# Kernel tuning notes

Measured on AMD Instinct MI355X. Metric: run time of the kernel, lower is better.

## Reference

```python
import jax, jax.numpy as jnp
import numpy as np

B, N, E = 32, 256, 300   # batch, num hyperedges, word emb size
H, K = 256, 8            # nhidden, nhead
MARGIN = 0.2


def setup_inputs() -> dict:
    key = jax.random.key(0)
    ks = jax.random.split(key, 10)
    s_in = 1.0 / np.sqrt(E)
    s_h = 1.0 / np.sqrt(H)
    s_fc = 1.0 / np.sqrt(H * K)
    return {
        'he_anchor': jax.random.normal(ks[0], (B, N, E), jnp.float32),
        'he_pos': jax.random.normal(ks[1], (B, N, E), jnp.float32),
        'he_neg': jax.random.normal(ks[2], (B, N, E), jnp.float32),
        'W_a2h': jax.random.uniform(ks[3], (H, E), jnp.float32, -s_in, s_in),
        'b_a2h': jax.random.uniform(ks[4], (H,), jnp.float32, -s_in, s_in),
        'W_c2h': jax.random.uniform(ks[5], (H, E), jnp.float32, -s_in, s_in),
        'b_c2h': jax.random.uniform(ks[6], (H,), jnp.float32, -s_in, s_in),
        'W_att': jax.random.uniform(ks[7], (K, H), jnp.float32, -s_h, s_h),
        'b_att': jax.random.uniform(ks[8], (K,), jnp.float32, -s_h, s_h),
        'W_fc': jax.random.uniform(ks[9], (1, H * K), jnp.float32, -s_fc, s_fc),
        'b_fc': jnp.zeros((1,), jnp.float32),
    }


def _score(x, y, W_a2h, b_a2h, W_c2h, b_c2h, W_att, b_att, W_fc, b_fc):
    # a2h / c2h projections, then permute to [B, H, N]
    Aa = jnp.transpose(x @ W_a2h.T + b_a2h, (0, 2, 1))  # [B,H,N]
    Ac = jnp.transpose(y @ W_c2h.T + b_c2h, (0, 2, 1))  # [B,H,M]
    # h2att applied to the outer product Aa[b,h,n]*Ac[b,h,m]; fuse into one einsum
    logits = jnp.einsum('bhn,bhm,kh->bknm', Aa, Ac, W_att) + b_att[None, :, None, None]
    b_, k_, n_, m_ = logits.shape
    att = jax.nn.softmax(logits.reshape(b_, k_, n_ * m_), axis=-1).reshape(b_, k_, n_, m_)
    # per-head bilinear aggregation: out[b,k,h] = sum_{n,m} Aa[b,h,n]*att[b,k,n,m]*Ac[b,h,m]
    t = jnp.einsum('bhn,bknm->bkhm', Aa, att)
    out = jnp.einsum('bkhm,bhm->bkh', t, Ac)
    # torch concat order is head-major: [B, K*H]
    out = out.reshape(b_, k_ * H)
    return out @ W_fc.T + b_fc  # [B,1]


def reference(he_anchor, he_pos, he_neg, W_a2h, b_a2h, W_c2h, b_c2h, W_att, b_att, W_fc, b_fc):
    score_p = _score(he_anchor, he_pos, W_a2h, b_a2h, W_c2h, b_c2h, W_att, b_att, W_fc, b_fc)
    score_n = _score(he_anchor, he_neg, W_a2h, b_a2h, W_c2h, b_c2h, W_att, b_att, W_fc, b_fc)
    loss = jnp.mean(jax.nn.relu(score_n - score_p + MARGIN))
    return loss
```

## Files before the change

kernel.cpp:

```cpp
#include <hip/hip_runtime.h>

#define BB 32
#define NN 256
#define EE 300
#define HH 256
#define KK 8
#define MARGINF 0.2f
#define EP 320

typedef __attribute__((ext_vector_type(8))) short bf16x8;
typedef __attribute__((ext_vector_type(4))) float f32x4;
typedef __attribute__((ext_vector_type(16))) float f32x16;

__device__ inline ushort f2bf(float f) {
  unsigned u = __float_as_uint(f);
  u += 0x7fffu + ((u >> 16) & 1u);
  return (ushort)(u >> 16);
}
__device__ inline float bf2f(ushort s) { return __uint_as_float(((unsigned)s) << 16); }
__device__ inline unsigned pack2bf(float f0, float f1) {
  unsigned u0 = __float_as_uint(f0); u0 += 0x7fffu + ((u0 >> 16) & 1u);
  unsigned u1 = __float_as_uint(f1); u1 += 0x7fffu + ((u1 >> 16) & 1u);
  return (u0 >> 16) | (u1 & 0xffff0000u);
}

__global__ __launch_bounds__(256) void wconv_kernel(
    const float* __restrict__ Wa, const float* __restrict__ Wc,
    ushort* __restrict__ Wb)
{
  const int i = blockIdx.x * 256 + threadIdx.x;
  const int e = i % EP;
  const int hw = i / EP;
  const int h = hw & 255;
  const int w = hw >> 8;
  const float* src = w ? Wc : Wa;
  Wb[i] = (e < EE) ? f2bf(src[(size_t)h * EE + e]) : (ushort)0;
}

__global__ __launch_bounds__(256, 3) void proj_kernel(
    const float* __restrict__ he_a, const float* __restrict__ he_p,
    const float* __restrict__ he_n, const ushort* __restrict__ Wb,
    const float* __restrict__ b_a2h, const float* __restrict__ b_c2h,
    ushort* __restrict__ AT)
{
  const int z = blockIdx.y;
  const int which = z >> 5;
  const int b = z & 31;
  const int n0 = blockIdx.x * 32;
  const int tid = threadIdx.x;
  const int wv = tid >> 6;
  const int lane = tid & 63;
  const int col = lane & 15;
  const int quad = lane >> 4;

  const float* X = (which == 0 ? he_a : which == 1 ? he_p : he_n) + (size_t)b * NN * EE;
  const ushort* W = Wb + (size_t)(which == 0 ? 0 : 1) * HH * EP;
  const float* bias = (which == 0 ? b_a2h : b_c2h);

  __shared__ __align__(16) ushort sX[32][328];
  __shared__ __align__(16) ushort tr[32][264];

  {
    const int row = tid >> 3, seg = tid & 7;
    const float* xr = X + (size_t)(n0 + row) * EE;
#pragma unroll
    for (int q = 0; q < 10; q++) {
      const int j = seg + 8 * q;
      float4 xv = {0.f, 0.f, 0.f, 0.f};
      if (j < 75) xv = *(const float4*)&xr[4 * j];
      uint2 p; p.x = pack2bf(xv.x, xv.y); p.y = pack2bf(xv.z, xv.w);
      *(uint2*)&sX[row][4 * j] = p;
    }
  }
  __syncthreads();

  f32x4 acc[2][4];
#pragma unroll
  for (int nf = 0; nf < 2; nf++)
#pragma unroll
    for (int mb = 0; mb < 4; mb++) acc[nf][mb] = (f32x4){0.f, 0.f, 0.f, 0.f};

#pragma unroll
  for (int ks = 0; ks < 10; ks++) {
    const int off = 32 * ks + 8 * quad;
    const bf16x8 a0 = *(const bf16x8*)&sX[col][off];
    const bf16x8 a1 = *(const bf16x8*)&sX[16 + col][off];
#pragma unroll
    for (int mb = 0; mb < 4; mb++) {
      const bf16x8 w8 = *(const bf16x8*)&W[(size_t)(64 * wv + 16 * mb + col) * EP + off];
      acc[0][mb] = __builtin_amdgcn_mfma_f32_16x16x32_bf16(a0, w8, acc[0][mb], 0, 0, 0);
      acc[1][mb] = __builtin_amdgcn_mfma_f32_16x16x32_bf16(a1, w8, acc[1][mb], 0, 0, 0);
    }
  }

#pragma unroll
  for (int nf = 0; nf < 2; nf++)
#pragma unroll
    for (int mb = 0; mb < 4; mb++) {
      const float bi = bias[64 * wv + 16 * mb + col];
#pragma unroll
      for (int r = 0; r < 4; r++)
        tr[16 * nf + 4 * quad + r][64 * wv + 16 * mb + col] = f2bf(acc[nf][mb][r] + bi);
    }
  __syncthreads();
  {
    const int row = tid >> 3, seg = tid & 7;
    ushort* dst = &AT[((size_t)(which * BB + b) * NN + n0 + row) * HH];
#pragma unroll
    for (int j = 0; j < 4; j++)
      *(uint4*)&dst[(seg * 4 + j) * 8] = *(const uint4*)&tr[row][(seg * 4 + j) * 8];
  }
}

__global__ __launch_bounds__(256, 2) void attn_kernel(
    const ushort* __restrict__ AT, const float* __restrict__ Watt,
    const float* __restrict__ Wfc, float* __restrict__ scoresK)
{
  const int idx = blockIdx.x;
  const int k = idx >> 6;
  const int g = idx & 63;
  const int which = g >> 5;
  const int b = g & 31;
  const int tid = threadIdx.x;
  const int wv = tid >> 6;
  const int lane = tid & 63;
  const int row32 = lane & 31;
  const int half32 = lane >> 5;

  const ushort* At_a = AT + (size_t)b * NN * HH;
  const ushort* At_c = AT + ((size_t)(1 + which) * BB + b) * NN * HH;
  const uint4* Ac_u4 = (const uint4*)At_c;

  __shared__ __align__(16) ushort sAc[64][264];
  __shared__ __align__(16) float wkf[256];
  __shared__ __align__(16) float wff[256];
  __shared__ float red[8];

  wkf[tid] = Watt[(size_t)k * HH + tid];
  wff[tid] = Wfc[(size_t)k * HH + tid];
  __syncthreads();

  float num = 0.f, den = 0.f;
  const int srow = tid >> 5, scol8 = (tid & 31) * 8;

  for (int s = 0; s < 2; s++) {
    const int nbase = 128 * s + 32 * wv;
    bf16x8 saf[16], gaf[16];
    const ushort* arow = At_a + (size_t)(nbase + row32) * HH;
#pragma unroll
    for (int ks = 0; ks < 16; ks++) {
      const int off = 16 * ks + 8 * half32;
      const bf16x8 a = *(const bf16x8*)&arow[off];
      const float4 wa = *(const float4*)&wkf[off];
      const float4 wb = *(const float4*)&wkf[off + 4];
      const float4 fa = *(const float4*)&wff[off];
      const float4 fb = *(const float4*)&wff[off + 4];
      const float w[8] = {wa.x, wa.y, wa.z, wa.w, wb.x, wb.y, wb.z, wb.w};
      const float f[8] = {fa.x, fa.y, fa.z, fa.w, fb.x, fb.y, fb.z, fb.w};
      union { bf16x8 v; unsigned u[4]; } sv, gv;
#pragma unroll
      for (int jj = 0; jj < 4; jj++) {
        const float a0 = bf2f((ushort)a[2 * jj]), a1 = bf2f((ushort)a[2 * jj + 1]);
        sv.u[jj] = pack2bf(a0 * w[2 * jj], a1 * w[2 * jj + 1]);
        gv.u[jj] = pack2bf(a0 * f[2 * jj], a1 * f[2 * jj + 1]);
      }
      saf[ks] = sv.v; gaf[ks] = gv.v;
    }

    for (int mc = 0; mc < 4; mc++) {
      __syncthreads();
#pragma unroll
      for (int q = 0; q < 8; q++) {
        const int row = q * 8 + srow;
        *(uint4*)&sAc[row][scol8] = Ac_u4[(size_t)(64 * mc + row) * 32 + (tid & 31)];
      }
      __syncthreads();

      f32x16 aS0 = {0,0,0,0,0,0,0,0,0,0,0,0,0,0,0,0};
      f32x16 aS1 = {0,0,0,0,0,0,0,0,0,0,0,0,0,0,0,0};
      f32x16 aG0 = {0,0,0,0,0,0,0,0,0,0,0,0,0,0,0,0};
      f32x16 aG1 = {0,0,0,0,0,0,0,0,0,0,0,0,0,0,0,0};
#pragma unroll
      for (int ks = 0; ks < 16; ks++) {
        const int off = 16 * ks + 8 * half32;
        const bf16x8 b0 = *(const bf16x8*)&sAc[row32][off];
        const bf16x8 b1 = *(const bf16x8*)&sAc[32 + row32][off];
        aS0 = __builtin_amdgcn_mfma_f32_32x32x16_bf16(saf[ks], b0, aS0, 0, 0, 0);
        aG0 = __builtin_amdgcn_mfma_f32_32x32x16_bf16(gaf[ks], b0, aG0, 0, 0, 0);
        aS1 = __builtin_amdgcn_mfma_f32_32x32x16_bf16(saf[ks], b1, aS1, 0, 0, 0);
        aG1 = __builtin_amdgcn_mfma_f32_32x32x16_bf16(gaf[ks], b1, aG1, 0, 0, 0);
      }
#pragma unroll
      for (int r = 0; r < 16; r++) {
        const float p0 = __expf(aS0[r]);
        den += p0; num += p0 * aG0[r];
        const float p1 = __expf(aS1[r]);
        den += p1; num += p1 * aG1[r];
      }
    }
  }

#pragma unroll
  for (int off = 32; off >= 1; off >>= 1) {
    num += __shfl_xor(num, off);
    den += __shfl_xor(den, off);
  }
  if (lane == 0) { red[wv] = num; red[4 + wv] = den; }
  __syncthreads();
  if (tid == 0) {
    const float nt = red[0] + red[1] + red[2] + red[3];
    const float dt = red[4] + red[5] + red[6] + red[7];
    scoresK[idx] = nt / dt;
  }
}

__global__ __launch_bounds__(64) void loss_kernel(
    const float* __restrict__ scoresK, const float* __restrict__ bfc,
    float* __restrict__ out)
{
  const int tid = threadIdx.x;
  float s = bfc[0];
#pragma unroll
  for (int k = 0; k < KK; k++) s += scoresK[k * 64 + tid];
  const float other = __shfl(s, tid + 32);
  float v = 0.f;
  if (tid < 32) v = fmaxf(other - s + MARGINF, 0.f);
#pragma unroll
  for (int off = 32; off >= 1; off >>= 1) v += __shfl_xor(v, off);
  if (tid == 0) out[0] = v * (1.0f / 32.0f);
}

extern "C" void kernel_launch(void* const* d_in, const int* in_sizes, int n_in,
                              void* d_out, int out_size, void* d_ws, size_t ws_size,
                              hipStream_t stream) {
  const float* he_a  = (const float*)d_in[0];
  const float* he_p  = (const float*)d_in[1];
  const float* he_n  = (const float*)d_in[2];
  const float* W_a2h = (const float*)d_in[3];
  const float* b_a2h = (const float*)d_in[4];
  const float* W_c2h = (const float*)d_in[5];
  const float* b_c2h = (const float*)d_in[6];
  const float* W_att = (const float*)d_in[7];
  const float* W_fc  = (const float*)d_in[9];
  const float* b_fc  = (const float*)d_in[10];

  ushort* AT = (ushort*)d_ws;
  float* scoresK = (float*)(AT + (size_t)3 * BB * NN * HH);
  ushort* Wb = (ushort*)(scoresK + 512);
  (void)ws_size; (void)in_sizes; (void)n_in; (void)out_size;

  wconv_kernel<<<640, 256, 0, stream>>>(W_a2h, W_c2h, Wb);
  dim3 pg(8, 96);
  proj_kernel<<<pg, 256, 0, stream>>>(he_a, he_p, he_n, Wb, b_a2h, b_c2h, AT);
  attn_kernel<<<512, 256, 0, stream>>>(AT, W_att, W_fc, scoresK);
  loss_kernel<<<1, 64, 0, stream>>>(scoresK, b_fc, (float*)d_out);
}
```

Measured before the change: 148.0 us.

## Switch attention operands to fp16, prefetch Ac tiles, and swap loop order

Stores the projected activations as fp16 instead of bf16 and uses f16 MFMA, so the per-head scaling of the anchor rows becomes packed half-precision vector multiplies rather than float unpack, multiply and repack. The loop order is inverted so each Ac chunk is loaded into shared memory once while the anchor fragments are rebuilt per chunk. The next chunk is prefetched into registers during compute, and the softmax accumulators are split in two to shorten dependency chains. This costs extra global reads of the anchor rows and more register pressure, and fp16 range or precision could differ from bf16 for larger logits.

```diff
diff --git a/kernel.cpp b/kernel.cpp
--- a/kernel.cpp
+++ b/kernel.cpp
@@ -9,6 +9,7 @@
 #define EP 320
 
 typedef __attribute__((ext_vector_type(8))) short bf16x8;
+typedef __attribute__((ext_vector_type(8))) _Float16 f16x8;
 typedef __attribute__((ext_vector_type(4))) float f32x4;
 typedef __attribute__((ext_vector_type(16))) float f32x16;
 
@@ -17,7 +18,6 @@
   u += 0x7fffu + ((u >> 16) & 1u);
   return (ushort)(u >> 16);
 }
-__device__ inline float bf2f(ushort s) { return __uint_as_float(((unsigned)s) << 16); }
 __device__ inline unsigned pack2bf(float f0, float f1) {
   unsigned u0 = __float_as_uint(f0); u0 += 0x7fffu + ((u0 >> 16) & 1u);
   unsigned u1 = __float_as_uint(f1); u1 += 0x7fffu + ((u1 >> 16) & 1u);
@@ -41,7 +41,7 @@
     const float* __restrict__ he_a, const float* __restrict__ he_p,
     const float* __restrict__ he_n, const ushort* __restrict__ Wb,
     const float* __restrict__ b_a2h, const float* __restrict__ b_c2h,
-    ushort* __restrict__ AT)
+    _Float16* __restrict__ AT)
 {
   const int z = blockIdx.y;
   const int which = z >> 5;
@@ -58,7 +58,7 @@
   const float* bias = (which == 0 ? b_a2h : b_c2h);
 
   __shared__ __align__(16) ushort sX[32][328];
-  __shared__ __align__(16) ushort tr[32][264];
+  __shared__ __align__(16) _Float16 tr[32][264];
 
   {
     const int row = tid >> 3, seg = tid & 7;
@@ -100,12 +100,12 @@
       const float bi = bias[64 * wv + 16 * mb + col];
 #pragma unroll
       for (int r = 0; r < 4; r++)
-        tr[16 * nf + 4 * quad + r][64 * wv + 16 * mb + col] = f2bf(acc[nf][mb][r] + bi);
+        tr[16 * nf + 4 * quad + r][64 * wv + 16 * mb + col] = (_Float16)(acc[nf][mb][r] + bi);
     }
   __syncthreads();
   {
     const int row = tid >> 3, seg = tid & 7;
-    ushort* dst = &AT[((size_t)(which * BB + b) * NN + n0 + row) * HH];
+    _Float16* dst = &AT[((size_t)(which * BB + b) * NN + n0 + row) * HH];
 #pragma unroll
     for (int j = 0; j < 4; j++)
       *(uint4*)&dst[(seg * 4 + j) * 8] = *(const uint4*)&tr[row][(seg * 4 + j) * 8];
@@ -113,7 +113,7 @@
 }
 
 __global__ __launch_bounds__(256, 2) void attn_kernel(
-    const ushort* __restrict__ AT, const float* __restrict__ Watt,
+    const _Float16* __restrict__ AT, const float* __restrict__ Watt,
     const float* __restrict__ Wfc, float* __restrict__ scoresK)
 {
   const int idx = blockIdx.x;
@@ -127,54 +127,53 @@
   const int row32 = lane & 31;
   const int half32 = lane >> 5;
 
-  const ushort* At_a = AT + (size_t)b * NN * HH;
-  const ushort* At_c = AT + ((size_t)(1 + which) * BB + b) * NN * HH;
+  const _Float16* At_a = AT + (size_t)b * NN * HH;
+  const _Float16* At_c = AT + ((size_t)(1 + which) * BB + b) * NN * HH;
   const uint4* Ac_u4 = (const uint4*)At_c;
 
-  __shared__ __align__(16) ushort sAc[64][264];
-  __shared__ __align__(16) float wkf[256];
-  __shared__ __align__(16) float wff[256];
+  __shared__ __align__(16) _Float16 sAc[64][264];
+  __shared__ __align__(16) _Float16 wkh[256];
+  __shared__ __align__(16) _Float16 wfh[256];
   __shared__ float red[8];
 
-  wkf[tid] = Watt[(size_t)k * HH + tid];
-  wff[tid] = Wfc[(size_t)k * HH + tid];
-  __syncthreads();
-
-  float num = 0.f, den = 0.f;
+  wkh[tid] = (_Float16)Watt[(size_t)k * HH + tid];
+  wfh[tid] = (_Float16)Wfc[(size_t)k * HH + tid];
+  __syncthreads();
+
+  float num0 = 0.f, den0 = 0.f, num1 = 0.f, den1 = 0.f;
   const int srow = tid >> 5, scol8 = (tid & 31) * 8;
 
-  for (int s = 0; s < 2; s++) {
-    const int nbase = 128 * s + 32 * wv;
-    bf16x8 saf[16], gaf[16];
-    const ushort* arow = At_a + (size_t)(nbase + row32) * HH;
-#pragma unroll
-    for (int ks = 0; ks < 16; ks++) {
-      const int off = 16 * ks + 8 * half32;
-      const bf16x8 a = *(const bf16x8*)&arow[off];
-      const float4 wa = *(const float4*)&wkf[off];
-      const float4 wb = *(const float4*)&wkf[off + 4];
-      const float4 fa = *(const float4*)&wff[off];
-      const float4 fb = *(const float4*)&wff[off + 4];
-      const float w[8] = {wa.x, wa.y, wa.z, wa.w, wb.x, wb.y, wb.z, wb.w};
-      const float f[8] = {fa.x, fa.y, fa.z, fa.w, fb.x, fb.y, fb.z, fb.w};
-      union { bf16x8 v; unsigned u[4]; } sv, gv;
-#pragma unroll
-      for (int jj = 0; jj < 4; jj++) {
-        const float a0 = bf2f((ushort)a[2 * jj]), a1 = bf2f((ushort)a[2 * jj + 1]);
-        sv.u[jj] = pack2bf(a0 * w[2 * jj], a1 * w[2 * jj + 1]);
-        gv.u[jj] = pack2bf(a0 * f[2 * jj], a1 * f[2 * jj + 1]);
+  uint4 pf[8];
+#pragma unroll
+  for (int q = 0; q < 8; q++)
+    pf[q] = Ac_u4[(size_t)(q * 8 + srow) * 32 + (tid & 31)];
+
+  for (int mc = 0; mc < 4; mc++) {
+    __syncthreads();
+#pragma unroll
+    for (int q = 0; q < 8; q++)
+      *(uint4*)&sAc[q * 8 + srow][scol8] = pf[q];
+    __syncthreads();
+    if (mc < 3) {
+#pragma unroll
+      for (int q = 0; q < 8; q++)
+        pf[q] = Ac_u4[(size_t)(64 * (mc + 1) + q * 8 + srow) * 32 + (tid & 31)];
+    }
+
+#pragma unroll 1
+    for (int s = 0; s < 2; s++) {
+      const int nbase = 128 * s + 32 * wv;
+      f16x8 saf[16], gaf[16];
+      const _Float16* arow = At_a + (size_t)(nbase + row32) * HH;
+#pragma unroll
+      for (int ks = 0; ks < 16; ks++) {
+        const int off = 16 * ks + 8 * half32;
+        const f16x8 a = *(const f16x8*)&arow[off];
+        const f16x8 w = *(const f16x8*)&wkh[off];
+        const f16x8 f = *(const f16x8*)&wfh[off];
+        saf[ks] = a * w;
+        gaf[ks] = a * f;
       }
-      saf[ks] = sv.v; gaf[ks] = gv.v;
-    }
-
-    for (int mc = 0; mc < 4; mc++) {
-      __syncthreads();
-#pragma unroll
-      for (int q = 0; q < 8; q++) {
-        const int row = q * 8 + srow;
-        *(uint4*)&sAc[row][scol8] = Ac_u4[(size_t)(64 * mc + row) * 32 + (tid & 31)];
-      }
-      __syncthreads();
 
       f32x16 aS0 = {0,0,0,0,0,0,0,0,0,0,0,0,0,0,0,0};
       f32x16 aS1 = {0,0,0,0,0,0,0,0,0,0,0,0,0,0,0,0};
@@ -183,23 +182,28 @@
 #pragma unroll
       for (int ks = 0; ks < 16; ks++) {
         const int off = 16 * ks + 8 * half32;
-        const bf16x8 b0 = *(const bf16x8*)&sAc[row32][off];
-        const bf16x8 b1 = *(const bf16x8*)&sAc[32 + row32][off];
-        aS0 = __builtin_amdgcn_mfma_f32_32x32x16_bf16(saf[ks], b0, aS0, 0, 0, 0);
-        aG0 = __builtin_amdgcn_mfma_f32_32x32x16_bf16(gaf[ks], b0, aG0, 0, 0, 0);
-        aS1 = __builtin_amdgcn_mfma_f32_32x32x16_bf16(saf[ks], b1, aS1, 0, 0, 0);
-        aG1 = __builtin_amdgcn_mfma_f32_32x32x16_bf16(gaf[ks], b1, aG1, 0, 0, 0);
+        const f16x8 b0 = *(const f16x8*)&sAc[row32][off];
+        const f16x8 b1 = *(const f16x8*)&sAc[32 + row32][off];
+        aS0 = __builtin_amdgcn_mfma_f32_32x32x16_f16(saf[ks], b0, aS0, 0, 0, 0);
+        aG0 = __builtin_amdgcn_mfma_f32_32x32x16_f16(gaf[ks], b0, aG0, 0, 0, 0);
+        aS1 = __builtin_amdgcn_mfma_f32_32x32x16_f16(saf[ks], b1, aS1, 0, 0, 0);
+        aG1 = __builtin_amdgcn_mfma_f32_32x32x16_f16(gaf[ks], b1, aG1, 0, 0, 0);
       }
 #pragma unroll
-      for (int r = 0; r < 16; r++) {
-        const float p0 = __expf(aS0[r]);
-        den += p0; num += p0 * aG0[r];
-        const float p1 = __expf(aS1[r]);
-        den += p1; num += p1 * aG1[r];
+      for (int r = 0; r < 16; r += 2) {
+        const float p0a = __expf(aS0[r]);
+        den0 += p0a; num0 += p0a * aG0[r];
+        const float p0b = __expf(aS0[r + 1]);
+        den1 += p0b; num1 += p0b * aG0[r + 1];
+        const float p1a = __expf(aS1[r]);
+        den0 += p1a; num0 += p1a * aG1[r];
+        const float p1b = __expf(aS1[r + 1]);
+        den1 += p1b; num1 += p1b * aG1[r + 1];
       }
     }
   }
 
+  float num = num0 + num1, den = den0 + den1;
 #pragma unroll
   for (int off = 32; off >= 1; off >>= 1) {
     num += __shfl_xor(num, off);
@@ -244,7 +248,7 @@
   const float* W_fc  = (const float*)d_in[9];
   const float* b_fc  = (const float*)d_in[10];
 
-  ushort* AT = (ushort*)d_ws;
+  _Float16* AT = (_Float16*)d_ws;
   float* scoresK = (float*)(AT + (size_t)3 * BB * NN * HH);
   ushort* Wb = (ushort*)(scoresK + 512);
   (void)ws_size; (void)in_sizes; (void)n_in; (void)out_size;
```

New measurement: 251.5 us. +69.9%, slower.
